# Performance work log

Measured on AMD Instinct MI355X. Metric: run time of the kernel, lower is better.

Reference implementation:

```python
import jax, jax.numpy as jnp
import numpy as np

B, S, D, H = 2, 2048, 1024, 16
DH = D // H  # key_dim = embed_dim // num_heads
NEG = 1e9    # Keras masked-softmax adder magnitude
EPS = 1e-6


def setup_inputs() -> dict:
    key = jax.random.key(0)
    ks = jax.random.split(key, 6)
    sc = 1.0 / np.sqrt(D)
    return {
        "x": jax.random.normal(ks[0], (B, S, D), jnp.float32),
        "Wq": jax.random.normal(ks[1], (D, H, DH), jnp.float32) * sc,
        "bq": jnp.zeros((H, DH), jnp.float32),
        "Wk": jax.random.normal(ks[2], (D, H, DH), jnp.float32) * sc,
        "bk": jnp.zeros((H, DH), jnp.float32),
        "Wv": jax.random.normal(ks[3], (D, H, DH), jnp.float32) * sc,
        "bv": jnp.zeros((H, DH), jnp.float32),
        "Wo": jax.random.normal(ks[4], (H, DH, D), jnp.float32) * (1.0 / np.sqrt(D)),
        "bo": jnp.zeros((D,), jnp.float32),
        "gamma": jnp.ones((D,), jnp.float32),
        "beta": jnp.zeros((D,), jnp.float32),
    }


def reference(x, Wq, bq, Wk, bk, Wv, bv, Wo, bo, gamma, beta):
    # Keras MultiHeadAttention(query=x, value=x), inference (dropouts are identity)
    q = jnp.einsum("bsd,dhk->bshk", x, Wq) + bq  # [B,S,H,DH]
    k = jnp.einsum("bsd,dhk->bshk", x, Wk) + bk
    v = jnp.einsum("bsd,dhk->bshk", x, Wv) + bv

    scores = jnp.einsum("bqhd,bkhd->bhqk", q, k) / jnp.sqrt(jnp.asarray(DH, x.dtype))
    # Source: mask = 1 - band_part(ones, -1, 0) -> ones strictly ABOVE diagonal.
    # Keras attends where mask==1 and adds (1-mask)*(-1e9) elsewhere. Faithful:
    i = jnp.arange(S)[:, None]
    j = jnp.arange(S)[None, :]
    allowed = (j > i).astype(scores.dtype)  # [S,S], strict upper triangle
    scores = scores + (allowed - 1.0) * NEG  # subtract 1e9 where not allowed
    probs = jax.nn.softmax(scores, axis=-1)

    ctx = jnp.einsum("bhqk,bkhd->bqhd", probs, v)  # [B,S,H,DH]
    attn_out = jnp.einsum("bqhd,hdo->bqo", ctx, Wo) + bo  # [B,S,D]

    # residual + LayerNorm(eps=1e-6)
    y = x + attn_out
    mu = jnp.mean(y, axis=-1, keepdims=True)
    var = jnp.mean(jnp.square(y - mu), axis=-1, keepdims=True)
    return (y - mu) * jax.lax.rsqrt(var + EPS) * gamma + beta
```

## Files before the change

kernel.cpp:

```cpp
#include <hip/hip_runtime.h>
#include <hip/hip_bf16.h>

typedef __hip_bfloat16 bf16;
typedef __attribute__((ext_vector_type(8))) short bf16x8;
typedef __attribute__((ext_vector_type(4))) float f32x4;

constexpr int Bc  = 2;
constexpr int Sc  = 2048;
constexpr int Dc  = 1024;
constexpr int Hc  = 16;
constexpr int DHc = 64;
constexpr int BS  = Bc * Sc;
constexpr int NT  = Sc / 64;

__device__ __forceinline__ float bs2f(unsigned short u) {
    union { unsigned int i; float f; } v; v.i = ((unsigned int)u) << 16; return v.f;
}
__device__ __forceinline__ short f2bs(float x) {
    bf16 h = __float2bfloat16(x);
    return *reinterpret_cast<short*>(&h);
}

typedef const __attribute__((address_space(1))) unsigned int* as1_u32p;
typedef __attribute__((address_space(3))) unsigned int* as3_u32p;
__device__ __forceinline__ void gl_lds16(const void* g, void* l) {
    __builtin_amdgcn_global_load_lds((as1_u32p)g, (as3_u32p)l, 16, 0, 0);
}

__global__ __launch_bounds__(256) void cast_x(const float* __restrict__ in,
                                              short* __restrict__ out) {
    const int i = (blockIdx.x * 256 + threadIdx.x) * 4;
    const float4 v = *(const float4*)(in + i);
    ushort4 o;
    o.x = (unsigned short)f2bs(v.x);
    o.y = (unsigned short)f2bs(v.y);
    o.z = (unsigned short)f2bs(v.z);
    o.w = (unsigned short)f2bs(v.w);
    *(ushort4*)(out + i) = o;
}

__global__ __launch_bounds__(256) void transpose_cast(
    const float* __restrict__ w0, const float* __restrict__ w1,
    const float* __restrict__ w2, const float* __restrict__ w3,
    short* __restrict__ outbase)
{
    __shared__ float T[64][65];
    const int z = blockIdx.z;
    const float* in = (z == 0) ? w0 : (z == 1) ? w1 : (z == 2) ? w2 : w3;
    short* out = outbase + (size_t)z * 1024 * 1024;
    const int k0 = blockIdx.x * 64, n0 = blockIdx.y * 64;
    const int t = threadIdx.x;
    #pragma unroll
    for (int it = 0; it < 4; ++it) {
        const int s = it * 256 + t;
        const int r = s >> 4, c = (s & 15) * 4;
        *(float4*)&T[r][c] = *(const float4*)(in + (size_t)(k0 + r) * 1024 + n0 + c);
    }
    __syncthreads();
    #pragma unroll
    for (int it = 0; it < 4; ++it) {
        const int s = it * 256 + t;
        const int rr = s >> 4, cc = (s & 15) * 4;
        ushort4 o;
        o.x = (unsigned short)f2bs(T[cc + 0][rr]);
        o.y = (unsigned short)f2bs(T[cc + 1][rr]);
        o.z = (unsigned short)f2bs(T[cc + 2][rr]);
        o.w = (unsigned short)f2bs(T[cc + 3][rr]);
        *(ushort4*)(out + (size_t)(n0 + rr) * 1024 + k0 + cc) = o;
    }
}

__global__ __launch_bounds__(256, 3) void gemm_bt(
    const short* __restrict__ A, const short* __restrict__ BTbase,
    const float* __restrict__ b0, const float* __restrict__ b1,
    const float* __restrict__ b2, short* __restrict__ Cbase)
{
    __shared__ __align__(16) short As[128 * 64];
    __shared__ __align__(16) short Bs[128 * 64];

    const int z = blockIdx.z;
    const short* BT = BTbase + (size_t)z * 1024 * 1024;
    const float* bias = (z == 0) ? b0 : (z == 1) ? b1 : b2;
    short* C = Cbase + (size_t)z * BS * Dc;

    const int t = threadIdx.x;
    const int lane = t & 63, w = t >> 6;
    const int quad = lane >> 4, l16 = lane & 15;
    const int wm = (w & 1) * 64, wn = (w >> 1) * 64;
    const int row0 = blockIdx.y * 128;
    const int col0 = blockIdx.x * 128;
    const int sw = l16 & 7;

    f32x4 acc[4][4] = {};

    for (int kt = 0; kt < 1024; kt += 64) {
        __syncthreads();
        #pragma unroll
        for (int i = 0; i < 4; ++i) {
            const int f = i * 256 + t;
            const int r = f >> 3;
            const int g = (f & 7) ^ (r & 7);
            short* lb = &As[(i * 256 + w * 64) * 8];
            gl_lds16(A + (size_t)(row0 + r) * 1024 + kt + g * 8, lb);
            short* lb2 = &Bs[(i * 256 + w * 64) * 8];
            gl_lds16(BT + (size_t)(col0 + r) * 1024 + kt + g * 8, lb2);
        }
        __syncthreads();
        #pragma unroll
        for (int ks = 0; ks < 2; ++ks) {
            bf16x8 av[4], bv[4];
            #pragma unroll
            for (int mt = 0; mt < 4; ++mt) {
                const int r = wm + mt * 16 + l16;
                av[mt] = *(const bf16x8*)&As[r * 64 + ((ks * 4 + quad) ^ sw) * 8];
            }
            #pragma unroll
            for (int nt = 0; nt < 4; ++nt) {
                const int r = wn + nt * 16 + l16;
                bv[nt] = *(const bf16x8*)&Bs[r * 64 + ((ks * 4 + quad) ^ sw) * 8];
            }
            #pragma unroll
            for (int mt = 0; mt < 4; ++mt)
                #pragma unroll
                for (int nt = 0; nt < 4; ++nt)
                    acc[mt][nt] = __builtin_amdgcn_mfma_f32_16x16x32_bf16(
                        av[mt], bv[nt], acc[mt][nt], 0, 0, 0);
        }
    }

    float bvv[4];
    #pragma unroll
    for (int nt = 0; nt < 4; ++nt) bvv[nt] = bias[col0 + wn + nt * 16 + l16];
    #pragma unroll
    for (int mt = 0; mt < 4; ++mt)
        #pragma unroll
        for (int reg = 0; reg < 4; ++reg) {
            const size_t row = row0 + wm + mt * 16 + quad * 4 + reg;
            #pragma unroll
            for (int nt = 0; nt < 4; ++nt) {
                const int col = col0 + wn + nt * 16 + l16;
                C[row * 1024 + col] = f2bs(acc[mt][nt][reg] + bvv[nt]);
            }
        }
}


template<bool DIAG>
__device__ __forceinline__ void qtile_step(
    const bf16x8 (&qf)[2],
    const short (&Ks)[64][72], const short (&VsT)[64][72],
    short (&Psw)[16][72],
    const int k0, const int row_base,
    const int quad, const int l16,
    float (&l)[4], f32x4 (&O)[4])
{
    bf16x8 kf[2][4];
    #pragma unroll
    for (int ks = 0; ks < 2; ++ks)
        #pragma unroll
        for (int nt = 0; nt < 4; ++nt)
            kf[ks][nt] = *(const bf16x8*)&Ks[nt * 16 + l16][ks * 32 + quad * 8];

    f32x4 S[4] = {};
    #pragma unroll
    for (int ks = 0; ks < 2; ++ks)
        #pragma unroll
        for (int nt = 0; nt < 4; ++nt)
            S[nt] = __builtin_amdgcn_mfma_f32_16x16x32_bf16(qf[ks], kf[ks][nt], S[nt], 0, 0, 0);

    #pragma unroll
    for (int nt = 0; nt < 4; ++nt) {
        #pragma unroll
        for (int reg = 0; reg < 4; ++reg) {
            float s = fminf(S[nt][reg] * 0.18033688f, 115.4f);
            if (DIAG) {
                const int col = k0 + nt * 16 + l16;
                const int row = row_base + quad * 4 + reg;
                s = (col > row) ? s : -126.0f;
            }
            const float p = exp2f(s);
            S[nt][reg] = p;
            l[reg] += p;
        }
    }

    #pragma unroll
    for (int reg = 0; reg < 4; ++reg) {
        const __hip_bfloat162 lo = __float22bfloat162_rn(make_float2(S[0][reg], S[1][reg]));
        const __hip_bfloat162 hi = __float22bfloat162_rn(make_float2(S[2][reg], S[3][reg]));
        uint2 u;
        u.x = *reinterpret_cast<const unsigned int*>(&lo);
        u.y = *reinterpret_cast<const unsigned int*>(&hi);
        *(uint2*)&Psw[quad * 4 + reg][l16 * 4] = u;
    }

    #pragma unroll
    for (int ks = 0; ks < 2; ++ks) {
        const bf16x8 pf = *(const bf16x8*)&Psw[l16][ks * 32 + quad * 8];
        #pragma unroll
        for (int nt = 0; nt < 4; ++nt) {
            const bf16x8 vf = *(const bf16x8*)&VsT[nt * 16 + l16][ks * 32 + quad * 8];
            O[nt] = __builtin_amdgcn_mfma_f32_16x16x32_bf16(pf, vf, O[nt], 0, 0, 0);
        }
    }
}

__global__ __launch_bounds__(256, 3) void attn_mfma(
    const short* __restrict__ Qg, const short* __restrict__ Kg,
    const short* __restrict__ Vg, short* __restrict__ CTX)
{
    __shared__ __align__(16) short Ks [2][64][72];
    __shared__ __align__(16) short VsT[2][64][72];
    __shared__ __align__(16) short Ps[4][16][72];

    const int tid  = threadIdx.x;
    const int lane = tid & 63, w = tid >> 6;
    const int quad = lane >> 4, l16 = lane & 15;
    const int p  = blockIdx.x;
    const int h  = blockIdx.y;
    const int b  = blockIdx.z;
    const size_t rb = (size_t)b * Sc;
    const int cb = h * DHc;

    const int skey = tid & 63, sseg = (tid >> 6) * 8;
    const int pkey = ((skey & 15) << 2) | (skey >> 4);

    #pragma unroll 1
    for (int ph = 0; ph < 2; ++ph) {
        const int myq = ph ? (NT - 1 - p) : p;
        const int t0  = myq;
        const int q0  = myq * 64;

        bf16x8 qf[2];
        {
            const short* qp = Qg + (rb + q0 + w * 16 + l16) * (size_t)Dc + cb + quad * 8;
            qf[0] = *(const bf16x8*)(qp);
            qf[1] = *(const bf16x8*)(qp + 32);
        }
        float l[4] = {};
        f32x4 O[4] = {};

        if (ph) __syncthreads();

        {
            const int buf = t0 & 1;
            const size_t g = (rb + t0 * 64 + skey) * (size_t)Dc + cb + sseg;
            const bf16x8 k0v = *(const bf16x8*)(Kg + g);
            const bf16x8 k1v = *(const bf16x8*)(Kg + g + 32);
            const bf16x8 v0v = *(const bf16x8*)(Vg + g);
            const bf16x8 v1v = *(const bf16x8*)(Vg + g + 32);
            *(bf16x8*)&Ks[buf][skey][sseg]      = k0v;
            *(bf16x8*)&Ks[buf][skey][sseg + 32] = k1v;
            #pragma unroll
            for (int e = 0; e < 8; ++e) {
                VsT[buf][sseg + e][pkey]      = v0v[e];
                VsT[buf][sseg + 32 + e][pkey] = v1v[e];
            }
        }
        __syncthreads();

        for (int t = t0; t < NT; ++t) {
            const int cur = t & 1;
            const bool havenext = (t + 1 < NT);
            bf16x8 pk0, pk1, pv0, pv1;
            if (havenext) {
                const size_t g = (rb + (t + 1) * 64 + skey) * (size_t)Dc + cb + sseg;
                pk0 = *(const bf16x8*)(Kg + g);
                pk1 = *(const bf16x8*)(Kg + g + 32);
                pv0 = *(const bf16x8*)(Vg + g);
                pv1 = *(const bf16x8*)(Vg + g + 32);
            }

            if (t == t0)
                qtile_step<true >(qf, Ks[cur], VsT[cur], Ps[w],
                                  t * 64, q0 + w * 16, quad, l16, l, O);
            else
                qtile_step<false>(qf, Ks[cur], VsT[cur], Ps[w],
                                  t * 64, q0 + w * 16, quad, l16, l, O);

            if (havenext) {
                const int nb = cur ^ 1;
                *(bf16x8*)&Ks[nb][skey][sseg]      = pk0;
                *(bf16x8*)&Ks[nb][skey][sseg + 32] = pk1;
                #pragma unroll
                for (int e = 0; e < 8; ++e) {
                    VsT[nb][sseg + e][pkey]      = pv0[e];
                    VsT[nb][sseg + 32 + e][pkey] = pv1[e];
                }
                __syncthreads();
            }
        }

        #pragma unroll
        for (int off = 1; off < 16; off <<= 1)
            #pragma unroll
            for (int reg = 0; reg < 4; ++reg)
                l[reg] += __shfl_xor(l[reg], off, 64);
        #pragma unroll
        for (int reg = 0; reg < 4; ++reg) l[reg] = 1.0f / l[reg];
        #pragma unroll
        for (int nt = 0; nt < 4; ++nt)
            #pragma unroll
            for (int reg = 0; reg < 4; ++reg) {
                const size_t row = rb + q0 + w * 16 + quad * 4 + reg;
                CTX[row * Dc + cb + nt * 16 + l16] = f2bs(O[nt][reg] * l[reg]);
            }
    }
}

__global__ __launch_bounds__(256) void vmean(const short* __restrict__ V,
                                             short* __restrict__ CTX)
{
    const int h = blockIdx.x, b = blockIdx.y;
    const int t = threadIdx.x;
    const int dh = t & 63, ck = t >> 6;
    float s = 0.f;
    const short* vp = V + ((size_t)b * Sc + ck * 512) * Dc + h * DHc + dh;
    for (int j = 0; j < 512; ++j) s += bs2f(vp[(size_t)j * Dc]);
    __shared__ float red[4][64];
    red[ck][dh] = s;
    __syncthreads();
    if (ck == 0) {
        const float tot = (red[0][dh] + red[1][dh] + red[2][dh] + red[3][dh]) * (1.f / Sc);
        CTX[((size_t)b * Sc + Sc - 1) * Dc + h * DHc + dh] = f2bs(tot);
    }
}

__global__ __launch_bounds__(256, 4) void resid_ln(
    const float* __restrict__ X, const short* __restrict__ AO,
    const float* __restrict__ gamma, const float* __restrict__ beta,
    float* __restrict__ out)
{
    const int r = blockIdx.x;
    const int t = threadIdx.x;
    const size_t base = (size_t)r * Dc + t * 4;

    const float4 x4 = *(const float4*)(X + base);
    const ushort4 a4 = *(const ushort4*)(AO + base);
    float y[4];
    y[0] = x4.x + bs2f(a4.x);
    y[1] = x4.y + bs2f(a4.y);
    y[2] = x4.z + bs2f(a4.z);
    y[3] = x4.w + bs2f(a4.w);

    float s  = y[0] + y[1] + y[2] + y[3];
    float s2 = y[0]*y[0] + y[1]*y[1] + y[2]*y[2] + y[3]*y[3];
    #pragma unroll
    for (int off = 1; off < 64; off <<= 1) {
        s  += __shfl_xor(s,  off, 64);
        s2 += __shfl_xor(s2, off, 64);
    }
    __shared__ float red[8];
    const int w = t >> 6;
    if ((t & 63) == 0) { red[w] = s; red[4 + w] = s2; }
    __syncthreads();
    s  = red[0] + red[1] + red[2] + red[3];
    s2 = red[4] + red[5] + red[6] + red[7];

    const float mu   = s * (1.0f / Dc);
    const float rstd = rsqrtf(s2 * (1.0f / Dc) - mu * mu + 1e-6f);

    const float4 g4 = *(const float4*)(gamma + t * 4);
    const float4 b4 = *(const float4*)(beta  + t * 4);
    float4 o;
    o.x = (y[0] - mu) * rstd * g4.x + b4.x;
    o.y = (y[1] - mu) * rstd * g4.y + b4.y;
    o.z = (y[2] - mu) * rstd * g4.z + b4.z;
    o.w = (y[3] - mu) * rstd * g4.w + b4.w;
    *(float4*)(out + base) = o;
}

extern "C" void kernel_launch(void* const* d_in, const int* in_sizes, int n_in,
                              void* d_out, int out_size, void* d_ws, size_t ws_size,
                              hipStream_t stream)
{
    (void)in_sizes; (void)n_in; (void)out_size; (void)ws_size;
    const float* x     = (const float*)d_in[0];
    const float* Wq    = (const float*)d_in[1];
    const float* bq    = (const float*)d_in[2];
    const float* Wk    = (const float*)d_in[3];
    const float* bk    = (const float*)d_in[4];
    const float* Wv    = (const float*)d_in[5];
    const float* bv    = (const float*)d_in[6];
    const float* Wo    = (const float*)d_in[7];
    const float* bo    = (const float*)d_in[8];
    const float* gamma = (const float*)d_in[9];
    const float* beta  = (const float*)d_in[10];
    float* out = (float*)d_out;

    const size_t matN = (size_t)BS * Dc;
    const size_t wN   = (size_t)Dc * Dc;
    short* xb = (short*)d_ws;
    short* WT = xb + matN;
    short* Qb = WT + 4 * wN;
    short* Kb = Qb + matN;
    short* Vb = Kb + matN;
    short* Cx = Vb + matN;
    short* AO = Qb;

    cast_x<<<matN / 1024, 256, 0, stream>>>(x, xb);

    dim3 gt(16, 16, 4);
    transpose_cast<<<gt, 256, 0, stream>>>(Wq, Wk, Wv, Wo, WT);

    dim3 gq(Dc / 128, BS / 128, 3);
    gemm_bt<<<gq, 256, 0, stream>>>(xb, WT, bq, bk, bv, Qb);

    dim3 ga(16, Hc, Bc);
    attn_mfma<<<ga, 256, 0, stream>>>(Qb, Kb, Vb, Cx);

    dim3 gv(Hc, Bc);
    vmean<<<gv, 256, 0, stream>>>(Vb, Cx);

    dim3 go(Dc / 128, BS / 128, 1);
    gemm_bt<<<go, 256, 0, stream>>>(Cx, WT + 3 * wN, bo, bo, bo, AO);

    resid_ln<<<BS, 256, 0, stream>>>(x, AO, gamma, beta, out);
}
```

Before: 221.6 us.

## Fold softmax scale into Q projection, compute row sums via MFMA, remap blocks

The softmax scale (log2e/sqrt(dh)) is now applied in the Q GEMM epilogue, which removes a multiply per score in attention. Row sums of P are accumulated with an extra MFMA against a ones vector instead of scalar adds plus a shuffle reduction. The change also adds s_setprio around the MFMA blocks, switches to incremental K/V pointer arithmetic, and remaps the block index so that blocks sharing an XCD get grouped heads. Rounding the scaled Q to bf16 alters numerics slightly, and the row sum is now taken over bf16-rounded probabilities.

Result: faster. 214.0 us (-3.4%).

```diff
diff --git a/kernel.cpp b/kernel.cpp
--- a/kernel.cpp
+++ b/kernel.cpp
@@ -73,7 +73,8 @@
 __global__ __launch_bounds__(256, 3) void gemm_bt(
     const short* __restrict__ A, const short* __restrict__ BTbase,
     const float* __restrict__ b0, const float* __restrict__ b1,
-    const float* __restrict__ b2, short* __restrict__ Cbase)
+    const float* __restrict__ b2, short* __restrict__ Cbase,
+    const float sc0)
 {
     __shared__ __align__(16) short As[128 * 64];
     __shared__ __align__(16) short Bs[128 * 64];
@@ -81,6 +82,7 @@
     const int z = blockIdx.z;
     const short* BT = BTbase + (size_t)z * 1024 * 1024;
     const float* bias = (z == 0) ? b0 : (z == 1) ? b1 : b2;
+    const float sc = (z == 0) ? sc0 : 1.0f;
     short* C = Cbase + (size_t)z * BS * Dc;
 
     const int t = threadIdx.x;
@@ -139,7 +141,7 @@
             #pragma unroll
             for (int nt = 0; nt < 4; ++nt) {
                 const int col = col0 + wn + nt * 16 + l16;
-                C[row * 1024 + col] = f2bs(acc[mt][nt][reg] + bvv[nt]);
+                C[row * 1024 + col] = f2bs((acc[mt][nt][reg] + bvv[nt]) * sc);
             }
         }
 }
@@ -152,7 +154,8 @@
     short (&Psw)[16][72],
     const int k0, const int row_base,
     const int quad, const int l16,
-    float (&l)[4], f32x4 (&O)[4])
+    const bf16x8 ones,
+    f32x4 &lacc, f32x4 (&O)[4])
 {
     bf16x8 kf[2][4];
     #pragma unroll
@@ -162,25 +165,25 @@
             kf[ks][nt] = *(const bf16x8*)&Ks[nt * 16 + l16][ks * 32 + quad * 8];
 
     f32x4 S[4] = {};
+    __builtin_amdgcn_s_setprio(1);
     #pragma unroll
     for (int ks = 0; ks < 2; ++ks)
         #pragma unroll
         for (int nt = 0; nt < 4; ++nt)
             S[nt] = __builtin_amdgcn_mfma_f32_16x16x32_bf16(qf[ks], kf[ks][nt], S[nt], 0, 0, 0);
+    __builtin_amdgcn_s_setprio(0);
 
     #pragma unroll
     for (int nt = 0; nt < 4; ++nt) {
         #pragma unroll
         for (int reg = 0; reg < 4; ++reg) {
-            float s = fminf(S[nt][reg] * 0.18033688f, 115.4f);
+            float s = fminf(S[nt][reg], 115.4f);
             if (DIAG) {
                 const int col = k0 + nt * 16 + l16;
                 const int row = row_base + quad * 4 + reg;
                 s = (col > row) ? s : -126.0f;
             }
-            const float p = exp2f(s);
-            S[nt][reg] = p;
-            l[reg] += p;
+            S[nt][reg] = exp2f(s);
         }
     }
 
@@ -194,15 +197,18 @@
         *(uint2*)&Psw[quad * 4 + reg][l16 * 4] = u;
     }
 
+    __builtin_amdgcn_s_setprio(1);
     #pragma unroll
     for (int ks = 0; ks < 2; ++ks) {
         const bf16x8 pf = *(const bf16x8*)&Psw[l16][ks * 32 + quad * 8];
+        lacc = __builtin_amdgcn_mfma_f32_16x16x32_bf16(pf, ones, lacc, 0, 0, 0);
         #pragma unroll
         for (int nt = 0; nt < 4; ++nt) {
             const bf16x8 vf = *(const bf16x8*)&VsT[nt * 16 + l16][ks * 32 + quad * 8];
             O[nt] = __builtin_amdgcn_mfma_f32_16x16x32_bf16(pf, vf, O[nt], 0, 0, 0);
         }
     }
+    __builtin_amdgcn_s_setprio(0);
 }
 
 __global__ __launch_bounds__(256, 3) void attn_mfma(
@@ -216,14 +222,23 @@
     const int tid  = threadIdx.x;
     const int lane = tid & 63, w = tid >> 6;
     const int quad = lane >> 4, l16 = lane & 15;
-    const int p  = blockIdx.x;
-    const int h  = blockIdx.y;
-    const int b  = blockIdx.z;
+
+    const int f  = blockIdx.x + 16 * blockIdx.y + 256 * blockIdx.z;
+    const int r_ = (f & 7) * 64 + (f >> 3);
+    const int p  = r_ & 15;
+    const int h  = (r_ >> 4) & 15;
+    const int b  = r_ >> 8;
     const size_t rb = (size_t)b * Sc;
     const int cb = h * DHc;
 
     const int skey = tid & 63, sseg = (tid >> 6) * 8;
     const int pkey = ((skey & 15) << 2) | (skey >> 4);
+
+    bf16x8 ones;
+    #pragma unroll
+    for (int e = 0; e < 8; ++e) ones[e] = (short)0x3F80;
+
+    const size_t tstride = (size_t)64 * Dc;
 
     #pragma unroll 1
     for (int ph = 0; ph < 2; ++ph) {
@@ -237,18 +252,20 @@
             qf[0] = *(const bf16x8*)(qp);
             qf[1] = *(const bf16x8*)(qp + 32);
         }
-        float l[4] = {};
+        f32x4 lacc = {};
         f32x4 O[4] = {};
+
+        const short* kp = Kg + (rb + (size_t)t0 * 64 + skey) * Dc + cb + sseg;
+        const short* vp = Vg + (rb + (size_t)t0 * 64 + skey) * Dc + cb + sseg;
 
         if (ph) __syncthreads();
 
         {
             const int buf = t0 & 1;
-            const size_t g = (rb + t0 * 64 + skey) * (size_t)Dc + cb + sseg;
-            const bf16x8 k0v = *(const bf16x8*)(Kg + g);
-            const bf16x8 k1v = *(const bf16x8*)(Kg + g + 32);
-            const bf16x8 v0v = *(const bf16x8*)(Vg + g);
-            const bf16x8 v1v = *(const bf16x8*)(Vg + g + 32);
+            const bf16x8 k0v = *(const bf16x8*)(kp);
+            const bf16x8 k1v = *(const bf16x8*)(kp + 32);
+            const bf16x8 v0v = *(const bf16x8*)(vp);
+            const bf16x8 v1v = *(const bf16x8*)(vp + 32);
             *(bf16x8*)&Ks[buf][skey][sseg]      = k0v;
             *(bf16x8*)&Ks[buf][skey][sseg + 32] = k1v;
             #pragma unroll
@@ -264,19 +281,18 @@
             const bool havenext = (t + 1 < NT);
             bf16x8 pk0, pk1, pv0, pv1;
             if (havenext) {
-                const size_t g = (rb + (t + 1) * 64 + skey) * (size_t)Dc + cb + sseg;
-                pk0 = *(const bf16x8*)(Kg + g);
-                pk1 = *(const bf16x8*)(Kg + g + 32);
-                pv0 = *(const bf16x8*)(Vg + g);
-                pv1 = *(const bf16x8*)(Vg + g + 32);
+                pk0 = *(const bf16x8*)(kp + tstride);
+                pk1 = *(const bf16x8*)(kp + tstride + 32);
+                pv0 = *(const bf16x8*)(vp + tstride);
+                pv1 = *(const bf16x8*)(vp + tstride + 32);
             }
 
             if (t == t0)
                 qtile_step<true >(qf, Ks[cur], VsT[cur], Ps[w],
-                                  t * 64, q0 + w * 16, quad, l16, l, O);
+                                  t * 64, q0 + w * 16, quad, l16, ones, lacc, O);
             else
                 qtile_step<false>(qf, Ks[cur], VsT[cur], Ps[w],
-                                  t * 64, q0 + w * 16, quad, l16, l, O);
+                                  t * 64, q0 + w * 16, quad, l16, ones, lacc, O);
 
             if (havenext) {
                 const int nb = cur ^ 1;
@@ -289,21 +305,19 @@
                 }
                 __syncthreads();
             }
-        }
-
-        #pragma unroll
-        for (int off = 1; off < 16; off <<= 1)
-            #pragma unroll
-            for (int reg = 0; reg < 4; ++reg)
-                l[reg] += __shfl_xor(l[reg], off, 64);
-        #pragma unroll
-        for (int reg = 0; reg < 4; ++reg) l[reg] = 1.0f / l[reg];
+            kp += tstride;
+            vp += tstride;
+        }
+
+        float inv[4];
+        #pragma unroll
+        for (int reg = 0; reg < 4; ++reg) inv[reg] = 1.0f / lacc[reg];
         #pragma unroll
         for (int nt = 0; nt < 4; ++nt)
             #pragma unroll
             for (int reg = 0; reg < 4; ++reg) {
                 const size_t row = rb + q0 + w * 16 + quad * 4 + reg;
-                CTX[row * Dc + cb + nt * 16 + l16] = f2bs(O[nt][reg] * l[reg]);
+                CTX[row * Dc + cb + nt * 16 + l16] = f2bs(O[nt][reg] * inv[reg]);
             }
     }
 }
@@ -404,16 +418,16 @@
     transpose_cast<<<gt, 256, 0, stream>>>(Wq, Wk, Wv, Wo, WT);
 
     dim3 gq(Dc / 128, BS / 128, 3);
-    gemm_bt<<<gq, 256, 0, stream>>>(xb, WT, bq, bk, bv, Qb);
-
-    dim3 ga(16, Hc, Bc);
+    gemm_bt<<<gq, 256, 0, stream>>>(xb, WT, bq, bk, bv, Qb, 0.18033688f);
+
+    dim3 ga(16, 16, 2);
     attn_mfma<<<ga, 256, 0, stream>>>(Qb, Kb, Vb, Cx);
 
     dim3 gv(Hc, Bc);
     vmean<<<gv, 256, 0, stream>>>(Vb, Cx);
 
     dim3 go(Dc / 128, BS / 128, 1);
-    gemm_bt<<<go, 256, 0, stream>>>(Cx, WT + 3 * wN, bo, bo, bo, AO);
+    gemm_bt<<<go, 256, 0, stream>>>(Cx, WT + 3 * wN, bo, bo, bo, AO, 1.0f);
 
     resid_ln<<<BS, 256, 0, stream>>>(x, AO, gamma, beta, out);
 }
```
